# Performance work log

Measured on AMD Instinct MI355X. Metric: run time of the kernel, lower is better.

Reference implementation:

```python
import jax, jax.numpy as jnp
import numpy as np

NBINS = 256
STRENGTH = 100.0
C, H, W = 64, 512, 512


def setup_inputs() -> dict:
    key = jax.random.key(0)
    k1, k2, k3, k4 = jax.random.split(key, 4)
    inp = jax.random.uniform(k1, (1, C, H, W), dtype=jnp.float32)
    tgt = jax.random.uniform(k2, (1, C, H, W), dtype=jnp.float32)
    maskI = jax.random.randint(k3, (1, 1, H, W), 0, 2).astype(jnp.int32)
    maskJ = jax.random.randint(k4, (1, 1, H, W), 0, 2).astype(jnp.int32)
    return {"input": inp, "target": tgt, "maskI": maskI, "maskJ": maskJ}


def _hist_remap(I, J, mI, mJ):
    # I, J: [c, HW] float; mI, mJ: [HW] {0,1} float
    c, hw = I.shape
    nI = mI.sum()
    nJ = mJ.sum()
    big = jnp.float32(1e30)
    # per-channel min/max of masked target values (J[mJ].view(c, nJ).min/max)
    minJ = jnp.min(jnp.where(mJ > 0, J, big), axis=1)   # [c]
    maxJ = jnp.max(jnp.where(mJ > 0, J, -big), axis=1)  # [c]
    step = (maxJ - minJ) / NBINS                          # [c]
    # masked per-channel histogram of target (cu.histogram), scaled by nI/nJ
    binJ = jnp.clip(jnp.floor((J - minJ[:, None]) / jnp.maximum(step[:, None], 1e-12)),
                    0, NBINS - 1).astype(jnp.int32)
    seg = binJ + jnp.arange(c, dtype=jnp.int32)[:, None] * NBINS
    hisJ = jax.ops.segment_sum(jnp.broadcast_to(mJ, (c, hw)).reshape(-1),
                               seg.reshape(-1), num_segments=c * NBINS).reshape(c, NBINS)
    hisJ = hisJ * (nI / nJ)
    cumJ = jnp.cumsum(hisJ, axis=1)                       # [c, nbins]
    # mask input; unmasked pixels -> -1 so they sort to the front (msk_sub trick)
    _I = I * mI - (1.0 - mI)                              # [c, HW]
    idxI = jnp.argsort(_I, axis=1)                        # ascending sort order
    # 1-indexed rank among the nI masked pixels (unmasked ranks <= 0, ignored later)
    rank = jnp.arange(hw, dtype=jnp.float32) - (hw - nI) + 1.0  # [HW]

    def per_ch(cum, his, r, mn, st):
        # CDF inverse: smallest bin b with cum[b] >= rank (cu.hist_remap2)
        b = jnp.clip(jnp.searchsorted(cum, r, side='left'), 0, NBINS - 1)
        lo = cum[b] - his[b]
        ratio = jnp.clip((r - lo) / jnp.maximum(his[b], 1e-12), 0.0, 1.0)
        return mn + (b.astype(jnp.float32) + ratio) * st

    vals = jax.vmap(per_ch)(cumJ, hisJ, jnp.broadcast_to(rank, (c, hw)), minJ, step)  # [c, HW]
    # scatter remapped sorted values back to original pixel positions
    R_sorted = jax.vmap(lambda idx, v: jnp.zeros(hw, dtype=v.dtype).at[idx].set(v))(idxI, vals)
    R = jnp.where(mI > 0, R_sorted, I)
    return R


def reference(input, target, maskI, maskJ):
    _, c, h, w = input.shape
    hw = h * w
    I = input[0].reshape(c, hw)
    J = target[0].reshape(c, hw)
    mI = maskI[0, 0].reshape(hw).astype(jnp.float32)
    mJ = maskJ[0, 0].reshape(hw).astype(jnp.float32)
    R = _hist_remap(I, J, mI, mJ)
    # F.mse_loss(I, R) * strength
    loss = jnp.mean((I - R) ** 2) * STRENGTH
    return loss
```

## Files before the change

### kernel.cpp

```cpp
#include <hip/hip_runtime.h>


#define CN    64
#define HWN   262144
#define NB    256
#define NBUK  8192
#define NBLK  16
#define BPIX  (HWN/NBLK)
#define PT    512
#define K1B   256
#define K1PIX (HWN/K1B)
#define GBUK  (NBUK/NBLK)
#define FXS2  268435456.0f
#define FXSI2 (1.0/268435456.0)

__global__ __launch_bounds__(512) void k_prep(
    const float* __restrict__ J, const int* __restrict__ mI,
    const int* __restrict__ mJ, unsigned* __restrict__ bIw,
    unsigned* __restrict__ bJw, unsigned* __restrict__ mnp2,
    unsigned* __restrict__ mxp2, double* __restrict__ lossacc,
    unsigned* __restrict__ donecnt)
{
  const int b = blockIdx.x, tid = threadIdx.x;
  __shared__ unsigned sbJ[K1PIX/32];
  if(tid < 32){
    const int4* mi4 = (const int4*)mI + (size_t)b*(K1PIX/4) + tid*8;
    const int4* mj4 = (const int4*)mJ + (size_t)b*(K1PIX/4) + tid*8;
    unsigned wi = 0u, wj = 0u;
    #pragma unroll
    for(int k = 0; k < 8; k++){
      int4 x = mi4[k];
      wi |= (unsigned)((x.x>0)|((x.y>0)<<1)|((x.z>0)<<2)|((x.w>0)<<3)) << (k*4);
      int4 y = mj4[k];
      wj |= (unsigned)((y.x>0)|((y.y>0)<<1)|((y.z>0)<<2)|((y.w>0)<<3)) << (k*4);
    }
    bIw[b*32 + tid] = wi;
    bJw[b*32 + tid] = wj;
    sbJ[tid] = wj;
  }
  if(b == 0 && tid == 0){ *lossacc = 0.0; *donecnt = 0u; }
  __syncthreads();
  const int grp = tid >> 6, lane = tid & 63;
  #pragma unroll
  for(int pass = 0; pass < 8; pass++){
    const int c = pass*8 + grp;
    const float4* Jc = (const float4*)(J + (size_t)c*HWN + (size_t)b*K1PIX);
    unsigned mn = 0x7F800000u, mx = 0u;
    #pragma unroll
    for(int k = 0; k < 4; k++){
      float4 v = Jc[k*64 + lane];
      unsigned b4 = (sbJ[k*8 + (lane>>3)] >> ((lane&7)*4)) & 0xFu;
      if(b4 & 1u){unsigned u=__float_as_uint(v.x); mn=min(mn,u); mx=max(mx,u);}
      if(b4 & 2u){unsigned u=__float_as_uint(v.y); mn=min(mn,u); mx=max(mx,u);}
      if(b4 & 4u){unsigned u=__float_as_uint(v.z); mn=min(mn,u); mx=max(mx,u);}
      if(b4 & 8u){unsigned u=__float_as_uint(v.w); mn=min(mn,u); mx=max(mx,u);}
    }
    for(int o = 32; o > 0; o >>= 1){
      mn = min(mn, (unsigned)__shfl_down(mn, o, 64));
      mx = max(mx, (unsigned)__shfl_down(mx, o, 64));
    }
    if(lane == 0){ mnp2[c*K1B + b] = mn; mxp2[c*K1B + b] = mx; }
  }
}

__device__ __forceinline__ void px_i(float v, float& qacc, unsigned& ci,
                                     unsigned* buk){
  int k = (int)(v * (float)NBUK);
  if(k > NBUK-1) k = NBUK-1;
  float dv = v - ((float)k + 0.5f) * (1.0f/(float)NBUK);
  int fx = (int)rintf(dv * FXS2);
  atomicAdd(&buk[k], ((unsigned)fx << 12) + 1u);
  qacc += dv*dv;
  ci++;
}

__global__ __launch_bounds__(PT, 2) void k_p1h(
    const float* __restrict__ I, const float* __restrict__ J,
    const unsigned* __restrict__ bIw, const unsigned* __restrict__ bJw,
    const unsigned* __restrict__ mnp2, const unsigned* __restrict__ mxp2,
    unsigned* __restrict__ pc, unsigned* __restrict__ qtot,
    unsigned* __restrict__ hisPart, unsigned* __restrict__ cp,
    double* __restrict__ qp)
{
  const int c = blockIdx.y, q = blockIdx.x, tid = threadIdx.x;
  const int bid = c*NBLK + q;
  const int wid = tid >> 6, lane = tid & 63;
  __shared__ unsigned buk[NBUK];
  __shared__ unsigned smbI[BPIX/32], smbJ[BPIX/32];
  __shared__ unsigned h2[2][NB];
  __shared__ double   dred[PT/64];
  __shared__ unsigned uci[PT/64], ucj[PT/64];
  __shared__ unsigned rmn[4], rmx[4];
  __shared__ float sh_mn, sh_den;
  for(int i = tid; i < NBUK; i += PT) buk[i] = 0u;
  smbI[tid] = bIw[q*512 + tid];
  smbJ[tid] = bJw[q*512 + tid];
  if(tid < NB){ h2[0][tid] = 0u; h2[1][tid] = 0u; }
  if(tid < K1B){
    unsigned mn = mnp2[c*K1B + tid];
    unsigned mx = mxp2[c*K1B + tid];
    for(int o = 32; o > 0; o >>= 1){
      mn = min(mn, (unsigned)__shfl_down(mn, o, 64));
      mx = max(mx, (unsigned)__shfl_down(mx, o, 64));
    }
    if(lane == 0){ rmn[wid] = mn; rmx[wid] = mx; }
  }
  __syncthreads();
  if(tid == 0){
    unsigned mn = min(min(rmn[0],rmn[1]), min(rmn[2],rmn[3]));
    unsigned mx = max(max(rmx[0],rmx[1]), max(rmx[2],rmx[3]));
    float mnv = __uint_as_float(mn);
    sh_mn  = mnv;
    sh_den = fmaxf((__uint_as_float(mx) - mnv) / (float)NB, 1e-12f);
  }
  __syncthreads();

  const float4* Ic = (const float4*)(I + (size_t)c*HWN + (size_t)q*BPIX);
  const float4* Jc = (const float4*)(J + (size_t)c*HWN + (size_t)q*BPIX);
  const float mnv = sh_mn, den = sh_den;
  float qacc = 0.0f;
  unsigned ci = 0, cj = 0;
  const int nsh = (tid & 7) * 4;
  const int bw  = tid >> 3;
  unsigned* hh = h2[wid & 1];

  float4 pi[2], pj[2];
  pi[0] = Ic[tid]; pj[0] = Jc[tid];
  #pragma unroll
  for(int g = 0; g < 8; g++){
    const int cur = g & 1, nxt = cur ^ 1;
    if(g < 7){ pi[nxt] = Ic[(g+1)*PT + tid]; pj[nxt] = Jc[(g+1)*PT + tid]; }
    const unsigned bitsI = (smbI[g*64 + bw] >> nsh) & 0xFu;
    const unsigned bitsJ = (smbJ[g*64 + bw] >> nsh) & 0xFu;
    float4 vi = pi[cur], vj = pj[cur];
    if(bitsI & 1u) px_i(vi.x, qacc, ci, buk);
    if(bitsI & 2u) px_i(vi.y, qacc, ci, buk);
    if(bitsI & 4u) px_i(vi.z, qacc, ci, buk);
    if(bitsI & 8u) px_i(vi.w, qacc, ci, buk);
    if(bitsJ & 1u){ float bf = floorf((vj.x - mnv)/den);
      bf = fminf(fmaxf(bf,0.0f),255.0f); atomicAdd(&hh[(int)bf],1u); cj++; }
    if(bitsJ & 2u){ float bf = floorf((vj.y - mnv)/den);
      bf = fminf(fmaxf(bf,0.0f),255.0f); atomicAdd(&hh[(int)bf],1u); cj++; }
    if(bitsJ & 4u){ float bf = floorf((vj.z - mnv)/den);
      bf = fminf(fmaxf(bf,0.0f),255.0f); atomicAdd(&hh[(int)bf],1u); cj++; }
    if(bitsJ & 8u){ float bf = floorf((vj.w - mnv)/den);
      bf = fminf(fmaxf(bf,0.0f),255.0f); atomicAdd(&hh[(int)bf],1u); cj++; }
  }
  __syncthreads();
  { unsigned* pcb = pc + (size_t)bid * NBUK;
    for(int i = tid; i < NBUK; i += PT) pcb[i] = buk[i]; }
  if(tid < NB) hisPart[(size_t)bid*NB + tid] = h2[0][tid] + h2[1][tid];

  { unsigned csum = 0;
    #pragma unroll
    for(int j = 0; j < 16; j++) csum += buk[tid*16 + j] & 0xFFFu;
    csum += __shfl_down(csum, 16, 64);
    csum += __shfl_down(csum,  8, 64);
    csum += __shfl_down(csum,  4, 64);
    csum += __shfl_down(csum,  2, 64);
    csum += __shfl_down(csum,  1, 64);
    if((tid & 31) == 0) qtot[bid*16 + (tid >> 5)] = csum;
  }

  double qd = (double)qacc;
  for(int o = 32; o > 0; o >>= 1){
    qd += __shfl_down(qd, o, 64);
    ci += __shfl_down(ci, o, 64);
    cj += __shfl_down(cj, o, 64);
  }
  if(lane == 0){ dred[wid] = qd; uci[wid] = ci; ucj[wid] = cj; }
  __syncthreads();
  if(tid == 0){
    double t = 0.0; unsigned aci = 0, acj = 0;
    for(int w = 0; w < PT/64; w++){ t += dred[w]; aci += uci[w]; acj += ucj[w]; }
    qp[bid] = t;
    if(c == 0){ cp[2*q] = aci; cp[2*q+1] = acj; }
  }
}

__global__ __launch_bounds__(512) void k_closs(
    const unsigned* __restrict__ pc, const unsigned* __restrict__ qtot,
    const unsigned* __restrict__ hisPart,
    const unsigned* __restrict__ mnp2, const unsigned* __restrict__ mxp2,
    const unsigned* __restrict__ cp, const double* __restrict__ qp,
    double* __restrict__ lossacc, unsigned* __restrict__ donecnt,
    float* __restrict__ out)
{
  const int c = blockIdx.y, qt = blockIdx.x, tid = threadIdx.x;
  const int wid = tid >> 6, lane = tid & 63;
  __shared__ unsigned hsum[NB], qsh[NB];
  __shared__ float cs[NB], hs[NB];
  __shared__ unsigned rmn[4], rmx[4], wsum[8];
  __shared__ double red2[8];
  __shared__ float sh_mn, sh_st;
  __shared__ unsigned sh_base;

  if(tid < K1B){
    unsigned mn = mnp2[c*K1B + tid];
    unsigned mx = mxp2[c*K1B + tid];
    for(int o = 32; o > 0; o >>= 1){
      mn = min(mn, (unsigned)__shfl_down(mn, o, 64));
      mx = max(mx, (unsigned)__shfl_down(mx, o, 64));
    }
    if(lane == 0){ rmn[wid] = mn; rmx[wid] = mx; }
  }
  if(tid < NB){
    unsigned hr = 0u;
    for(int xb = 0; xb < NBLK; xb++) hr += hisPart[(size_t)(c*NBLK + xb)*NB + tid];
    hsum[tid] = hr;
    qsh[tid]  = qtot[c*256 + tid];
  }
  __syncthreads();
  if(tid == 0){
    unsigned mn = min(min(rmn[0],rmn[1]), min(rmn[2],rmn[3]));
    unsigned mx = max(max(rmx[0],rmx[1]), max(rmx[2],rmx[3]));
    float mnv = __uint_as_float(mn);
    sh_mn = mnv;
    sh_st = (__uint_as_float(mx) - mnv) / (float)NB;
    unsigned ciw = 0, cjw = 0;
    for(int qi = 0; qi < NBLK; qi++){ ciw += cp[2*qi]; cjw += cp[2*qi+1]; }
    float ratio = (float)ciw / (float)cjw;
    float cum = 0.0f;
    for(int b = 0; b < NB; b++){
      float hh = (float)hsum[b] * ratio;
      hs[b] = hh;
      cum += hh;
      cs[b] = cum;
    }
    unsigned base = 0;
    for(int sl = 0; sl < NBLK; sl++)
      for(int g2 = 0; g2 < qt; g2++) base += qsh[sl*16 + g2];
    sh_base = base;
  }
  __syncthreads();

  unsigned  kk = 0;
  long long ss = 0;
  for(int sl = 0; sl < NBLK; sl++){
    unsigned w = pc[(size_t)(c*NBLK + sl)*NBUK + qt*GBUK + tid];
    kk += w & 0xFFFu;  ss += (int)w >> 12;
  }
  unsigned v = kk;
  for(int o = 1; o < 64; o <<= 1){
    unsigned t = __shfl_up(v, o, 64);
    if(lane >= o) v += t;
  }
  if(lane == 63) wsum[wid] = v;
  __syncthreads();
  unsigned wbase = 0;
  for(int w = 0; w < wid; w++) wbase += wsum[w];
  unsigned texcl = sh_base + wbase + (v - kk);

  float  mnvf = sh_mn, stepf = sh_st;
  double mnvd = (double)mnvf, stepd = (double)stepf;

  float rf0 = (float)(texcl + 1u);
  int lo = 0, hi = NB;
  while(lo < hi){ int mid = (lo + hi) >> 1; if(cs[mid] < rf0) lo = mid + 1; else hi = mid; }
  int bin = (lo > NB-1) ? NB-1 : lo;

  double acc = 0.0;
  if(kk){
    unsigned ra = texcl + 1u, rb = texcl + kk;
    double sval = 0.0;
    while(ra <= rb){
      while(bin < NB-1 && cs[bin] < (float)ra) bin++;
      float csb = cs[bin], hsb = hs[bin];
      unsigned re = (bin == NB-1) ? rb : min(rb, (unsigned)floorf(csb));
      double lovd = (double)csb - (double)hsb;
      double den2 = fmax((double)hsb, 1e-12);
      double ra_d = (double)ra, re_d = (double)re, nn = (double)(re - ra + 1u);
      double rta = (ra_d - lovd)/den2, rtb = (re_d - lovd)/den2;
      if(hsb > 0.0f && rta >= 0.0 && rtb <= 1.0){
        double sumr = 0.5*(ra_d + re_d)*nn;
        sval += nn*(mnvd + (double)bin*stepd) + stepd*(sumr - nn*lovd)/den2;
      } else {
        for(unsigned rr = ra; rr <= re; rr++){
          float rf = (float)rr;
          float lov = csb - hsb;
          float rt = (rf - lov) / fmaxf(hsb, 1e-12f);
          rt = fminf(fmaxf(rt, 0.0f), 1.0f);
          sval += (double)(mnvf + ((float)bin + rt)*stepf);
        }
      }
      ra = re + 1u;
    }
    double kb   = (double)kk;
    double cb   = ((double)(qt*GBUK + tid) + 0.5) * (1.0/(double)NBUK);
    double vbar = sval/kb - cb;
    double S    = (double)ss * FXSI2;
    acc = kb*vbar*vbar - 2.0*vbar*S;
  }
  if(qt == 0 && tid == 0){
    double qsum = 0.0;
    for(int qi = 0; qi < NBLK; qi++) qsum += qp[c*NBLK + qi];
    acc += qsum;
  }
  for(int o = 32; o > 0; o >>= 1) acc += __shfl_down(acc, o, 64);
  if(lane == 0) red2[wid] = acc;
  __syncthreads();
  if(tid == 0){
    double t = 0.0;
    for(int w = 0; w < 8; w++) t += red2[w];
    atomicAdd(lossacc, t);
    __threadfence();
    unsigned old = atomicAdd(donecnt, 1u);
    if(old == (unsigned)(CN*NBLK - 1)){
      double tot = atomicAdd(lossacc, 0.0);
      out[0] = (float)(tot * (100.0 / (double)((size_t)CN * HWN)));
    }
  }
}

extern "C" void kernel_launch(void* const* d_in, const int* in_sizes, int n_in,
                              void* d_out, int out_size, void* d_ws, size_t ws_size,
                              hipStream_t stream){
  const float* I  = (const float*)d_in[0];
  const float* J  = (const float*)d_in[1];
  const int*   mI = (const int*)d_in[2];
  const int*   mJ = (const int*)d_in[3];
  float* out = (float*)d_out;

  char* base = (char*)d_ws;
  size_t pcB = (size_t)CN * NBLK * NBUK * sizeof(unsigned);
  unsigned* pc      = (unsigned*)base;
  char* p = base + pcB;
  double*   qp      = (double*)p;   p += (size_t)CN*NBLK*sizeof(double);
  double*   lossacc = (double*)p;   p += sizeof(double);
  unsigned* hisPart = (unsigned*)p; p += (size_t)CN*NBLK*NB*sizeof(unsigned);
  unsigned* qtot    = (unsigned*)p; p += (size_t)CN*NBLK*16*sizeof(unsigned);
  unsigned* mnp2    = (unsigned*)p; p += (size_t)CN*K1B*sizeof(unsigned);
  unsigned* mxp2    = (unsigned*)p; p += (size_t)CN*K1B*sizeof(unsigned);
  unsigned* cp      = (unsigned*)p; p += 2*NBLK*sizeof(unsigned);
  unsigned* donecnt = (unsigned*)p; p += sizeof(unsigned);
  size_t off = (size_t)(p - base); off = (off + 15) & ~(size_t)15;
  unsigned* bIw = (unsigned*)(base + off);
  unsigned* bJw = bIw + HWN/32;

  k_prep<<<K1B, 512, 0, stream>>>(J, mI, mJ, bIw, bJw, mnp2, mxp2,
                                  lossacc, donecnt);
  k_p1h<<<dim3(NBLK, CN), PT, 0, stream>>>(I, J, bIw, bJw, mnp2, mxp2,
                                           pc, qtot, hisPart, cp, qp);
  k_closs<<<dim3(NBLK, CN), 512, 0, stream>>>(pc, qtot, hisPart, mnp2, mxp2,
                                              cp, qp, lossacc, donecnt, out);
}
```

Measured before the change: 206.7 us.

## Rebalance prep into mask-pack plus channel-grouped min/max blocks; finer closs grid

```diff
diff --git a/kernel.cpp b/kernel.cpp
--- a/kernel.cpp
+++ b/kernel.cpp
@@ -8,58 +8,69 @@
 #define NBLK  16
 #define BPIX  (HWN/NBLK)
 #define PT    512
-#define K1B   256
-#define K1PIX (HWN/K1B)
-#define GBUK  (NBUK/NBLK)
+#define MMS   64
+#define MMPIX (HWN/MMS)
+#define CLB   32
+#define CBUK  (NBUK/CLB)
 #define FXS2  268435456.0f
 #define FXSI2 (1.0/268435456.0)
 
 __global__ __launch_bounds__(512) void k_prep(
     const float* __restrict__ J, const int* __restrict__ mI,
-    const int* __restrict__ mJ, unsigned* __restrict__ bIw,
-    unsigned* __restrict__ bJw, unsigned* __restrict__ mnp2,
-    unsigned* __restrict__ mxp2, double* __restrict__ lossacc,
+    const int* __restrict__ mJ, unsigned char* __restrict__ bI,
+    unsigned char* __restrict__ bJ, unsigned* __restrict__ mnp,
+    unsigned* __restrict__ mxp, double* __restrict__ lossacc,
     unsigned* __restrict__ donecnt)
 {
-  const int b = blockIdx.x, tid = threadIdx.x;
-  __shared__ unsigned sbJ[K1PIX/32];
-  if(tid < 32){
-    const int4* mi4 = (const int4*)mI + (size_t)b*(K1PIX/4) + tid*8;
-    const int4* mj4 = (const int4*)mJ + (size_t)b*(K1PIX/4) + tid*8;
-    unsigned wi = 0u, wj = 0u;
-    #pragma unroll
-    for(int k = 0; k < 8; k++){
-      int4 x = mi4[k];
-      wi |= (unsigned)((x.x>0)|((x.y>0)<<1)|((x.z>0)<<2)|((x.w>0)<<3)) << (k*4);
-      int4 y = mj4[k];
-      wj |= (unsigned)((y.x>0)|((y.y>0)<<1)|((y.z>0)<<2)|((y.w>0)<<3)) << (k*4);
-    }
-    bIw[b*32 + tid] = wi;
-    bJw[b*32 + tid] = wj;
-    sbJ[tid] = wj;
-  }
-  if(b == 0 && tid == 0){ *lossacc = 0.0; *donecnt = 0u; }
-  __syncthreads();
-  const int grp = tid >> 6, lane = tid & 63;
+  const int bx = blockIdx.x, tid = threadIdx.x;
+  __shared__ unsigned smn[8][8], smx[8][8];
+  if(bx < 64){
+    const int t = bx*512 + tid;
+    const int4* a = (const int4*)mI + 2*t;
+    int4 x0 = a[0], x1 = a[1];
+    unsigned b = (unsigned)((x0.x>0)|((x0.y>0)<<1)|((x0.z>0)<<2)|((x0.w>0)<<3)
+               |((x1.x>0)<<4)|((x1.y>0)<<5)|((x1.z>0)<<6)|((x1.w>0)<<7));
+    const int4* cm = (const int4*)mJ + 2*t;
+    int4 y0 = cm[0], y1 = cm[1];
+    unsigned d = (unsigned)((y0.x>0)|((y0.y>0)<<1)|((y0.z>0)<<2)|((y0.w>0)<<3)
+               |((y1.x>0)<<4)|((y1.y>0)<<5)|((y1.z>0)<<6)|((y1.w>0)<<7));
+    bI[t] = (unsigned char)b;
+    bJ[t] = (unsigned char)d;
+    if(bx == 0 && tid == 0){ *lossacc = 0.0; *donecnt = 0u; }
+    return;
+  }
+  const int m = bx - 64, s = m >> 3, g = m & 7;
+  const int wid = tid >> 6, lane = tid & 63;
+  const int4* mj4 = (const int4*)mJ + s*(MMPIX/4);
+  int4 y0 = mj4[tid], y1 = mj4[512 + tid];
+  unsigned b40 = (unsigned)((y0.x>0)|((y0.y>0)<<1)|((y0.z>0)<<2)|((y0.w>0)<<3));
+  unsigned b41 = (unsigned)((y1.x>0)|((y1.y>0)<<1)|((y1.z>0)<<2)|((y1.w>0)<<3));
   #pragma unroll
-  for(int pass = 0; pass < 8; pass++){
-    const int c = pass*8 + grp;
-    const float4* Jc = (const float4*)(J + (size_t)c*HWN + (size_t)b*K1PIX);
+  for(int ch = 0; ch < 8; ch++){
+    const int c = g*8 + ch;
+    const float4* Jc = (const float4*)(J + (size_t)c*HWN + (size_t)s*MMPIX);
+    float4 v0 = Jc[tid], v1 = Jc[512 + tid];
     unsigned mn = 0x7F800000u, mx = 0u;
-    #pragma unroll
-    for(int k = 0; k < 4; k++){
-      float4 v = Jc[k*64 + lane];
-      unsigned b4 = (sbJ[k*8 + (lane>>3)] >> ((lane&7)*4)) & 0xFu;
-      if(b4 & 1u){unsigned u=__float_as_uint(v.x); mn=min(mn,u); mx=max(mx,u);}
-      if(b4 & 2u){unsigned u=__float_as_uint(v.y); mn=min(mn,u); mx=max(mx,u);}
-      if(b4 & 4u){unsigned u=__float_as_uint(v.z); mn=min(mn,u); mx=max(mx,u);}
-      if(b4 & 8u){unsigned u=__float_as_uint(v.w); mn=min(mn,u); mx=max(mx,u);}
-    }
+    if(b40&1u){unsigned u=__float_as_uint(v0.x); mn=min(mn,u); mx=max(mx,u);}
+    if(b40&2u){unsigned u=__float_as_uint(v0.y); mn=min(mn,u); mx=max(mx,u);}
+    if(b40&4u){unsigned u=__float_as_uint(v0.z); mn=min(mn,u); mx=max(mx,u);}
+    if(b40&8u){unsigned u=__float_as_uint(v0.w); mn=min(mn,u); mx=max(mx,u);}
+    if(b41&1u){unsigned u=__float_as_uint(v1.x); mn=min(mn,u); mx=max(mx,u);}
+    if(b41&2u){unsigned u=__float_as_uint(v1.y); mn=min(mn,u); mx=max(mx,u);}
+    if(b41&4u){unsigned u=__float_as_uint(v1.z); mn=min(mn,u); mx=max(mx,u);}
+    if(b41&8u){unsigned u=__float_as_uint(v1.w); mn=min(mn,u); mx=max(mx,u);}
     for(int o = 32; o > 0; o >>= 1){
       mn = min(mn, (unsigned)__shfl_down(mn, o, 64));
       mx = max(mx, (unsigned)__shfl_down(mx, o, 64));
     }
-    if(lane == 0){ mnp2[c*K1B + b] = mn; mxp2[c*K1B + b] = mx; }
+    if(lane == 0){ smn[wid][ch] = mn; smx[wid][ch] = mx; }
+  }
+  __syncthreads();
+  if(tid < 8){
+    unsigned mn = 0x7F800000u, mx = 0u;
+    for(int w = 0; w < 8; w++){ mn = min(mn, smn[w][tid]); mx = max(mx, smx[w][tid]); }
+    mnp[(g*8 + tid)*MMS + s] = mn;
+    mxp[(g*8 + tid)*MMS + s] = mx;
   }
 }
 
@@ -77,7 +88,7 @@
 __global__ __launch_bounds__(PT, 2) void k_p1h(
     const float* __restrict__ I, const float* __restrict__ J,
     const unsigned* __restrict__ bIw, const unsigned* __restrict__ bJw,
-    const unsigned* __restrict__ mnp2, const unsigned* __restrict__ mxp2,
+    const unsigned* __restrict__ mnp, const unsigned* __restrict__ mxp,
     unsigned* __restrict__ pc, unsigned* __restrict__ qtot,
     unsigned* __restrict__ hisPart, unsigned* __restrict__ cp,
     double* __restrict__ qp)
@@ -90,28 +101,23 @@
   __shared__ unsigned h2[2][NB];
   __shared__ double   dred[PT/64];
   __shared__ unsigned uci[PT/64], ucj[PT/64];
-  __shared__ unsigned rmn[4], rmx[4];
   __shared__ float sh_mn, sh_den;
   for(int i = tid; i < NBUK; i += PT) buk[i] = 0u;
   smbI[tid] = bIw[q*512 + tid];
   smbJ[tid] = bJw[q*512 + tid];
   if(tid < NB){ h2[0][tid] = 0u; h2[1][tid] = 0u; }
-  if(tid < K1B){
-    unsigned mn = mnp2[c*K1B + tid];
-    unsigned mx = mxp2[c*K1B + tid];
+  if(tid < MMS){
+    unsigned mn = mnp[c*MMS + tid];
+    unsigned mx = mxp[c*MMS + tid];
     for(int o = 32; o > 0; o >>= 1){
       mn = min(mn, (unsigned)__shfl_down(mn, o, 64));
       mx = max(mx, (unsigned)__shfl_down(mx, o, 64));
     }
-    if(lane == 0){ rmn[wid] = mn; rmx[wid] = mx; }
-  }
-  __syncthreads();
-  if(tid == 0){
-    unsigned mn = min(min(rmn[0],rmn[1]), min(rmn[2],rmn[3]));
-    unsigned mx = max(max(rmx[0],rmx[1]), max(rmx[2],rmx[3]));
-    float mnv = __uint_as_float(mn);
-    sh_mn  = mnv;
-    sh_den = fmaxf((__uint_as_float(mx) - mnv) / (float)NB, 1e-12f);
+    if(tid == 0){
+      float mnv = __uint_as_float(mn);
+      sh_mn  = mnv;
+      sh_den = fmaxf((__uint_as_float(mx) - mnv) / (float)NB, 1e-12f);
+    }
   }
   __syncthreads();
 
@@ -154,12 +160,11 @@
   { unsigned csum = 0;
     #pragma unroll
     for(int j = 0; j < 16; j++) csum += buk[tid*16 + j] & 0xFFFu;
-    csum += __shfl_down(csum, 16, 64);
-    csum += __shfl_down(csum,  8, 64);
-    csum += __shfl_down(csum,  4, 64);
-    csum += __shfl_down(csum,  2, 64);
-    csum += __shfl_down(csum,  1, 64);
-    if((tid & 31) == 0) qtot[bid*16 + (tid >> 5)] = csum;
+    csum += __shfl_down(csum, 8, 64);
+    csum += __shfl_down(csum, 4, 64);
+    csum += __shfl_down(csum, 2, 64);
+    csum += __shfl_down(csum, 1, 64);
+    if((tid & 15) == 0) qtot[bid*32 + (tid >> 4)] = csum;
   }
 
   double qd = (double)qacc;
@@ -178,45 +183,51 @@
   }
 }
 
-__global__ __launch_bounds__(512) void k_closs(
+__global__ __launch_bounds__(256) void k_closs(
     const unsigned* __restrict__ pc, const unsigned* __restrict__ qtot,
     const unsigned* __restrict__ hisPart,
-    const unsigned* __restrict__ mnp2, const unsigned* __restrict__ mxp2,
+    const unsigned* __restrict__ mnp, const unsigned* __restrict__ mxp,
     const unsigned* __restrict__ cp, const double* __restrict__ qp,
     double* __restrict__ lossacc, unsigned* __restrict__ donecnt,
     float* __restrict__ out)
 {
   const int c = blockIdx.y, qt = blockIdx.x, tid = threadIdx.x;
   const int wid = tid >> 6, lane = tid & 63;
-  __shared__ unsigned hsum[NB], qsh[NB];
+  __shared__ unsigned hsum[NB], qsh[NBLK*32];
   __shared__ float cs[NB], hs[NB];
-  __shared__ unsigned rmn[4], rmx[4], wsum[8];
-  __shared__ double red2[8];
+  __shared__ unsigned colsum[32], wsum[4];
+  __shared__ double red2[4];
   __shared__ float sh_mn, sh_st;
   __shared__ unsigned sh_base;
 
-  if(tid < K1B){
-    unsigned mn = mnp2[c*K1B + tid];
-    unsigned mx = mxp2[c*K1B + tid];
+  if(tid < MMS){
+    unsigned mn = mnp[c*MMS + tid];
+    unsigned mx = mxp[c*MMS + tid];
     for(int o = 32; o > 0; o >>= 1){
       mn = min(mn, (unsigned)__shfl_down(mn, o, 64));
       mx = max(mx, (unsigned)__shfl_down(mx, o, 64));
     }
-    if(lane == 0){ rmn[wid] = mn; rmx[wid] = mx; }
-  }
-  if(tid < NB){
-    unsigned hr = 0u;
+    if(tid == 0){
+      float mnv = __uint_as_float(mn);
+      sh_mn = mnv;
+      sh_st = (__uint_as_float(mx) - mnv) / (float)NB;
+    }
+  }
+  { unsigned hr = 0u;
+    #pragma unroll
     for(int xb = 0; xb < NBLK; xb++) hr += hisPart[(size_t)(c*NBLK + xb)*NB + tid];
-    hsum[tid] = hr;
-    qsh[tid]  = qtot[c*256 + tid];
+    hsum[tid] = hr; }
+  qsh[tid]       = qtot[c*NBLK*32 + tid];
+  qsh[tid + 256] = qtot[c*NBLK*32 + 256 + tid];
+  __syncthreads();
+  if(tid < 32){
+    unsigned csm = 0;
+    #pragma unroll
+    for(int sl = 0; sl < NBLK; sl++) csm += qsh[sl*32 + tid];
+    colsum[tid] = csm;
   }
   __syncthreads();
   if(tid == 0){
-    unsigned mn = min(min(rmn[0],rmn[1]), min(rmn[2],rmn[3]));
-    unsigned mx = max(max(rmx[0],rmx[1]), max(rmx[2],rmx[3]));
-    float mnv = __uint_as_float(mn);
-    sh_mn = mnv;
-    sh_st = (__uint_as_float(mx) - mnv) / (float)NB;
     unsigned ciw = 0, cjw = 0;
     for(int qi = 0; qi < NBLK; qi++){ ciw += cp[2*qi]; cjw += cp[2*qi+1]; }
     float ratio = (float)ciw / (float)cjw;
@@ -228,18 +239,26 @@
       cs[b] = cum;
     }
     unsigned base = 0;
-    for(int sl = 0; sl < NBLK; sl++)
-      for(int g2 = 0; g2 < qt; g2++) base += qsh[sl*16 + g2];
+    for(int g2 = 0; g2 < qt; g2++) base += colsum[g2];
     sh_base = base;
   }
   __syncthreads();
 
-  unsigned  kk = 0;
-  long long ss = 0;
-  for(int sl = 0; sl < NBLK; sl++){
-    unsigned w = pc[(size_t)(c*NBLK + sl)*NBUK + qt*GBUK + tid];
-    kk += w & 0xFFFu;  ss += (int)w >> 12;
-  }
+  unsigned kk0=0, kk1=0, kk2=0, kk3=0;
+  long long ss0=0, ss1=0, ss2=0, ss3=0;
+  #pragma unroll
+  for(int sl = 0; sl < NBLK; sl += 4){
+    unsigned w0 = pc[(size_t)(c*NBLK + sl    )*NBUK + qt*CBUK + tid];
+    unsigned w1 = pc[(size_t)(c*NBLK + sl + 1)*NBUK + qt*CBUK + tid];
+    unsigned w2 = pc[(size_t)(c*NBLK + sl + 2)*NBUK + qt*CBUK + tid];
+    unsigned w3 = pc[(size_t)(c*NBLK + sl + 3)*NBUK + qt*CBUK + tid];
+    kk0 += w0 & 0xFFFu;  ss0 += (int)w0 >> 12;
+    kk1 += w1 & 0xFFFu;  ss1 += (int)w1 >> 12;
+    kk2 += w2 & 0xFFFu;  ss2 += (int)w2 >> 12;
+    kk3 += w3 & 0xFFFu;  ss3 += (int)w3 >> 12;
+  }
+  unsigned  kk = kk0 + kk1 + kk2 + kk3;
+  long long ss = ss0 + ss1 + ss2 + ss3;
   unsigned v = kk;
   for(int o = 1; o < 64; o <<= 1){
     unsigned t = __shfl_up(v, o, 64);
@@ -286,7 +305,7 @@
       ra = re + 1u;
     }
     double kb   = (double)kk;
-    double cb   = ((double)(qt*GBUK + tid) + 0.5) * (1.0/(double)NBUK);
+    double cb   = ((double)(qt*CBUK + tid) + 0.5) * (1.0/(double)NBUK);
     double vbar = sval/kb - cb;
     double S    = (double)ss * FXSI2;
     acc = kb*vbar*vbar - 2.0*vbar*S;
@@ -301,11 +320,11 @@
   __syncthreads();
   if(tid == 0){
     double t = 0.0;
-    for(int w = 0; w < 8; w++) t += red2[w];
+    for(int w = 0; w < 4; w++) t += red2[w];
     atomicAdd(lossacc, t);
     __threadfence();
     unsigned old = atomicAdd(donecnt, 1u);
-    if(old == (unsigned)(CN*NBLK - 1)){
+    if(old == (unsigned)(CN*CLB - 1)){
       double tot = atomicAdd(lossacc, 0.0);
       out[0] = (float)(tot * (100.0 / (double)((size_t)CN * HWN)));
     }
@@ -328,19 +347,20 @@
   double*   qp      = (double*)p;   p += (size_t)CN*NBLK*sizeof(double);
   double*   lossacc = (double*)p;   p += sizeof(double);
   unsigned* hisPart = (unsigned*)p; p += (size_t)CN*NBLK*NB*sizeof(unsigned);
-  unsigned* qtot    = (unsigned*)p; p += (size_t)CN*NBLK*16*sizeof(unsigned);
-  unsigned* mnp2    = (unsigned*)p; p += (size_t)CN*K1B*sizeof(unsigned);
-  unsigned* mxp2    = (unsigned*)p; p += (size_t)CN*K1B*sizeof(unsigned);
+  unsigned* qtot    = (unsigned*)p; p += (size_t)CN*NBLK*32*sizeof(unsigned);
+  unsigned* mnp     = (unsigned*)p; p += (size_t)CN*MMS*sizeof(unsigned);
+  unsigned* mxp     = (unsigned*)p; p += (size_t)CN*MMS*sizeof(unsigned);
   unsigned* cp      = (unsigned*)p; p += 2*NBLK*sizeof(unsigned);
   unsigned* donecnt = (unsigned*)p; p += sizeof(unsigned);
   size_t off = (size_t)(p - base); off = (off + 15) & ~(size_t)15;
-  unsigned* bIw = (unsigned*)(base + off);
-  unsigned* bJw = bIw + HWN/32;
-
-  k_prep<<<K1B, 512, 0, stream>>>(J, mI, mJ, bIw, bJw, mnp2, mxp2,
+  unsigned char* bIb = (unsigned char*)(base + off);
+  unsigned char* bJb = bIb + HWN/8;
+
+  k_prep<<<576, 512, 0, stream>>>(J, mI, mJ, bIb, bJb, mnp, mxp,
                                   lossacc, donecnt);
-  k_p1h<<<dim3(NBLK, CN), PT, 0, stream>>>(I, J, bIw, bJw, mnp2, mxp2,
+  k_p1h<<<dim3(NBLK, CN), PT, 0, stream>>>(I, J, (const unsigned*)bIb,
+                                           (const unsigned*)bJb, mnp, mxp,
                                            pc, qtot, hisPart, cp, qp);
-  k_closs<<<dim3(NBLK, CN), 512, 0, stream>>>(pc, qtot, hisPart, mnp2, mxp2,
-                                              cp, qp, lossacc, donecnt, out);
-}
+  k_closs<<<dim3(CLB, CN), 256, 0, stream>>>(pc, qtot, hisPart, mnp, mxp,
+                                             cp, qp, lossacc, donecnt, out);
+}
```

New measurement: 217.6 us. +5.3%, slower.
